# Performance work log

Hardware: AMD Instinct MI355X
Metric: run time of the kernel (lower is better)

Reference implementation:

```python
import jax, jax.numpy as jnp
import numpy as np

B, S, D, F, E, K, H = 4, 1024, 512, 2048, 8, 2, 8
HEAD_DIM = D // H


def setup_inputs() -> dict:
    key = jax.random.key(0)
    ks = jax.random.split(key, 8)
    s = 0.02
    return {
        "x": jax.random.normal(ks[0], (B, S, D), jnp.float32),
        "gate_Wk": jax.random.normal(ks[1], (D, D), jnp.float32) * s,
        "gate_bk": jnp.zeros((D,), jnp.float32),
        "expert_queries": jax.random.normal(ks[2], (E, D), jnp.float32),
        "Wqkv": jax.random.normal(ks[3], (E, 3 * D, D), jnp.float32) * s,
        "bqkv": jnp.zeros((E, 3 * D), jnp.float32),
        "Wo": jax.random.normal(ks[4], (E, D, D), jnp.float32) * s,
        "bo": jnp.zeros((E, D), jnp.float32),
        "g1": jnp.ones((E, D), jnp.float32),
        "be1": jnp.zeros((E, D), jnp.float32),
        "W1": jax.random.normal(ks[5], (E, F, D), jnp.float32) * s,
        "bf1": jnp.zeros((E, F), jnp.float32),
        "W2": jax.random.normal(ks[6], (E, D, F), jnp.float32) * s,
        "bf2": jnp.zeros((E, D), jnp.float32),
        "g2": jnp.ones((E, D), jnp.float32),
        "be2": jnp.zeros((E, D), jnp.float32),
    }


def _layernorm(x, g, b):
    m = x.mean(-1, keepdims=True)
    v = ((x - m) ** 2).mean(-1, keepdims=True)
    return (x - m) * jax.lax.rsqrt(v + 1e-5) * g + b


def _expert(x, Wqkv, bqkv, Wo, bo, g1, be1, W1, bf1, W2, bf2, g2, be2):
    # x: [B,S,D]; one ExpertTransformerDecoder block (dropout=0, eval)
    b, s, d = x.shape
    qkv = x @ Wqkv.T + bqkv                      # [B,S,3D]
    q, k, v = jnp.split(qkv, 3, axis=-1)
    to_heads = lambda t: t.reshape(b, s, H, HEAD_DIM).transpose(0, 2, 1, 3)
    q, k, v = to_heads(q), to_heads(k), to_heads(v)
    scale = 1.0 / np.sqrt(HEAD_DIM).astype(np.float32)
    attn = jax.nn.softmax(jnp.einsum('bhqd,bhkd->bhqk', q * scale, k), axis=-1)
    ctx = jnp.einsum('bhqk,bhkd->bhqd', attn, v).transpose(0, 2, 1, 3).reshape(b, s, d)
    ctx = ctx @ Wo.T + bo
    x = _layernorm(x + ctx, g1, be1)
    h = jax.nn.gelu(x @ W1.T + bf1, approximate=False)
    h = jax.nn.gelu(h @ W2.T + bf2, approximate=False)
    return _layernorm(x + h, g2, be2)


def reference(x, gate_Wk, gate_bk, expert_queries, Wqkv, bqkv, Wo, bo,
              g1, be1, W1, bf1, W2, bf2, g2, be2):
    # attention gating: softmax over experts of <key_proj(x), expert_q> * d^-0.5
    keys = x @ gate_Wk.T + gate_bk                      # [B,S,D]
    scores = jnp.einsum('bsd,ed->bse', keys, expert_queries) * (D ** -0.5)
    probs = jax.nn.softmax(scores, axis=-1)             # [B,S,E]
    # top-k mask + renormalize
    _, idx = jax.lax.top_k(probs, K)                    # [B,S,K]
    mask = jax.nn.one_hot(idx, E, dtype=probs.dtype).sum(-2)
    gated = probs * mask
    gated = gated / (gated.sum(-1, keepdims=True) + 1e-9)
    # run all experts densely (as the torch code does), vmapped over E
    eo = jax.vmap(_expert, in_axes=(None,) + (0,) * 12)(
        x, Wqkv, bqkv, Wo, bo, g1, be1, W1, bf1, W2, bf2, g2, be2)  # [E,B,S,D]
    return jnp.einsum('ebsd,bse->bsd', eo, gated)
```

## Files before the change

kernel.cpp:

```cpp
#include <hip/hip_runtime.h>
#include <cstdint>
#include <cmath>

#define Bc 4
#define Sc 1024
#define Dc 512
#define Fc 2048
#define Ec 8
#define Hc 8
#define Mc 4096

typedef unsigned short u16;
typedef __attribute__((ext_vector_type(8))) short bf16x8;
typedef __attribute__((ext_vector_type(4))) float f32x4;

__device__ __forceinline__ float bf2f(u16 u) {
  unsigned v = ((unsigned)u) << 16;
  return __builtin_bit_cast(float, v);
}
__device__ __forceinline__ u16 f2bf(float f) {
  unsigned u = __builtin_bit_cast(unsigned, f);
  unsigned r = 0x7fffu + ((u >> 16) & 1u);
  return (u16)((u + r) >> 16);
}
__device__ __forceinline__ unsigned pack2bf(float a, float b) {
  return (unsigned)f2bf(a) | ((unsigned)f2bf(b) << 16);
}
__device__ __forceinline__ float gelu_f(float x) {
  const float z = 1.5957691216057308f * fmaf(0.044715f * x, x * x, x);
  const float e = __expf(z);
  return x * (1.0f - __builtin_amdgcn_rcpf(e + 1.0f));
}
__device__ __forceinline__ void async16(const void* g, void* l) {
  __builtin_amdgcn_global_load_lds(
      (const __attribute__((address_space(1))) unsigned int*)g,
      (__attribute__((address_space(3))) unsigned int*)l, 16, 0, 0);
}

__global__ __launch_bounds__(256) void cvt5_kernel(const float* __restrict__ p0, u16* __restrict__ q0,
                                                   const float* __restrict__ p1, u16* __restrict__ q1,
                                                   const float* __restrict__ p2, u16* __restrict__ q2,
                                                   const float* __restrict__ p3, u16* __restrict__ q3,
                                                   const float* __restrict__ p4, u16* __restrict__ q4) {
  int bx = blockIdx.x;
  const float* in;
  u16* outp;
  if (bx < 2048) { in = p0; outp = q0; }
  else if (bx < 8192) { in = p1; outp = q1; bx -= 2048; }
  else if (bx < 10240) { in = p2; outp = q2; bx -= 8192; }
  else if (bx < 18432) { in = p3; outp = q3; bx -= 10240; }
  else { in = p4; outp = q4; bx -= 18432; }
  const long long i = ((long long)bx * 256 + threadIdx.x) * 4;
  const float4 v = *(const float4*)(in + i);
  ushort4 o;
  o.x = f2bf(v.x); o.y = f2bf(v.y); o.z = f2bf(v.z); o.w = f2bf(v.w);
  *(ushort4*)(outp + i) = o;
}

__global__ __launch_bounds__(256) void weq_kernel(const float* __restrict__ gWk,
                                                  const float* __restrict__ eq,
                                                  float* __restrict__ weq) {
  __shared__ float red[4][64];
  const int tid = threadIdx.x, wave = tid >> 6, lane = tid & 63;
  const int d = blockIdx.x * 64 + lane;
  const int e = blockIdx.y;
  float acc = 0.f;
  for (int j = wave * 128; j < wave * 128 + 128; ++j)
    acc += gWk[(long long)j * 512 + d] * eq[e * 512 + j];
  red[wave][lane] = acc;
  __syncthreads();
  if (wave == 0)
    weq[e * 512 + d] = red[0][lane] + red[1][lane] + red[2][lane] + red[3][lane];
}
__global__ void beq_kernel(const float* __restrict__ gbk, const float* __restrict__ eq,
                           float* __restrict__ beq) {
  const int wave = threadIdx.x >> 6, lane = threadIdx.x & 63;
  for (int e = wave; e < 8; e += 4) {
    float a = 0.f;
#pragma unroll
    for (int i = 0; i < 8; ++i) a += gbk[lane + 64 * i] * eq[e * 512 + lane + 64 * i];
#pragma unroll
    for (int off = 32; off; off >>= 1) a += __shfl_xor(a, off);
    if (lane == 0) beq[e] = a;
  }
}

__global__ __launch_bounds__(256) void gate_kernel(const float* __restrict__ x,
                                                   const float* __restrict__ weq,
                                                   const float* __restrict__ beq,
                                                   float* __restrict__ gated,
                                                   int* __restrict__ cnt, int* __restrict__ tlist,
                                                   int* __restrict__ pos) {
  const int wave = threadIdx.x >> 6, lane = threadIdx.x & 63;
  const int t = blockIdx.x * 4 + wave;
  const float* xr = x + (long long)t * 512;
  float acc[8] = {};
#pragma unroll
  for (int i = 0; i < 8; ++i) {
    const float xv = xr[lane + 64 * i];
#pragma unroll
    for (int e2 = 0; e2 < 8; ++e2) acc[e2] += xv * weq[e2 * 512 + lane + 64 * i];
  }
#pragma unroll
  for (int e2 = 0; e2 < 8; ++e2)
#pragma unroll
    for (int off = 32; off; off >>= 1) acc[e2] += __shfl_xor(acc[e2], off);
  if (lane == 0) {
    const float scale = 0.044194173824159216f;
    float s[8], mx = -1e30f;
#pragma unroll
    for (int e2 = 0; e2 < 8; ++e2) { s[e2] = (acc[e2] + beq[e2]) * scale; mx = fmaxf(mx, s[e2]); }
    float p[8], sum = 0.f;
#pragma unroll
    for (int e2 = 0; e2 < 8; ++e2) { p[e2] = expf(s[e2] - mx); sum += p[e2]; }
#pragma unroll
    for (int e2 = 0; e2 < 8; ++e2) p[e2] /= sum;
    int i1 = 0;
#pragma unroll
    for (int e2 = 1; e2 < 8; ++e2) if (p[e2] > p[i1]) i1 = e2;
    int i2 = (i1 == 0) ? 1 : 0;
#pragma unroll
    for (int e2 = 0; e2 < 8; ++e2) if (e2 != i1 && e2 != i2 && p[e2] > p[i2]) i2 = e2;
    const float denom = p[i1] + p[i2] + 1e-9f;
#pragma unroll
    for (int e2 = 0; e2 < 8; ++e2)
      gated[t * 8 + e2] = (e2 == i1 || e2 == i2) ? p[e2] / denom : 0.f;
    const int b = t >> 10;
    int s1 = atomicAdd(cnt + i1 * 4 + b, 1);
    tlist[(i1 * 4 + b) * 1024 + s1] = t;
    pos[i1 * 4096 + t] = s1;
    int s2 = atomicAdd(cnt + i2 * 4 + b, 1);
    tlist[(i2 * 4 + b) * 1024 + s2] = t;
    pos[i2 * 4096 + t] = s2;
  }
}

__global__ void pad_kernel(const int* __restrict__ cnt, int* __restrict__ tlist) {
  const int seg = blockIdx.x;
  const int c = cnt[seg];
  const int ce = (c + 127) & ~127;
  const int tpad = (seg & 3) << 10;
  for (int i = c + (int)threadIdx.x; i < ce; i += 128) tlist[seg * 1024 + i] = tpad;
}

__global__ void wl_kernel(const int* __restrict__ cnt, int* __restrict__ wl) {
  const int seg = threadIdx.x;
  if (seg >= 32) return;
  int base = 0;
  for (int s = 0; s < seg; ++s) base += (cnt[s] + 127) >> 7;
  const int nt = (cnt[seg] + 127) >> 7;
  for (int t = 0; t < nt; ++t) wl[base + t] = (seg << 8) | t;
  for (int t = 0; t < 2 * nt; ++t) wl[128 + 2 * base + t] = (seg << 8) | t;
  if (seg == 31) { wl[96] = base + nt; wl[97] = 2 * (base + nt); }
}

template <int GELU, int QKV, int ROUTED, int BK, int GATHER>
__global__ __launch_bounds__(256) void gemm_bf16(
    const u16* __restrict__ A, const u16* __restrict__ Bw, const float* __restrict__ bias,
    u16* __restrict__ Cout, u16* __restrict__ vT, int M, int N, int K, long long Astride,
    long long Bstride, const int* __restrict__ wl, const int* __restrict__ tlist) {
  int e;
  long long bm;
  if (ROUTED) {
    const int total = wl[96];
    if ((int)blockIdx.x >= total) return;
    const int item = wl[blockIdx.x];
    const int seg = item >> 8, tile = item & 255;
    e = seg >> 2;
    bm = ((long long)(seg & 3) << 10) + tile * 128;
  } else {
    e = blockIdx.z;
    bm = (long long)blockIdx.x * 128;
  }
  __shared__ __attribute__((aligned(16))) u16 As[128 * BK];
  __shared__ __attribute__((aligned(16))) u16 Bs[128 * BK];
  const int tid = threadIdx.x;
  const int wave = tid >> 6, lane = tid & 63;
  const long long bn = (long long)blockIdx.y * 128;
  const u16* Ag = A + (long long)e * Astride + bm * K;
  const u16* Bg = Bw + ((long long)e * Bstride + bn) * K;
  constexpr int LPR = BK / 8;
  constexpr int RPI = 512 / BK;
  constexpr int IPW = BK / 16;
  const int lrow = lane / LPR, lpos = lane % LPR;
  const int lm = lane & 15, quad = lane >> 4;
  const int wm = (wave >> 1) * 64, wn = (wave & 1) * 64;
  int tok[IPW];
  if (GATHER) {
    const long long tbase = (long long)e * 4096 + bm;
#pragma unroll
    for (int i = 0; i < IPW; ++i) {
      const int gi = wave * IPW + i;
      tok[i] = tlist[tbase + gi * RPI + lrow];
    }
  }
  f32x4 acc[4][4] = {};
  for (int kk = 0; kk < K; kk += BK) {
    __syncthreads();
#pragma unroll
    for (int i = 0; i < IPW; ++i) {
      const int gi = wave * IPW + i;
      const int row = gi * RPI + lrow;
      const int sc = lpos ^ (row & 7);
      if (GATHER)
        async16(A + (long long)tok[i] * K + kk + sc * 8, &As[gi * 512]);
      else
        async16(Ag + (long long)row * K + kk + sc * 8, &As[gi * 512]);
      async16(Bg + (long long)row * K + kk + sc * 8, &Bs[gi * 512]);
    }
    __syncthreads();
#pragma unroll
    for (int ks = 0; ks < BK / 32; ++ks) {
      bf16x8 af[4], bfr[4];
#pragma unroll
      for (int mi = 0; mi < 4; ++mi) {
        const int row = wm + mi * 16 + lm;
        const int ch = (ks * 4 + quad) ^ (row & 7);
        af[mi] = *(const bf16x8*)(As + row * BK + ch * 8);
      }
#pragma unroll
      for (int nj = 0; nj < 4; ++nj) {
        const int row = wn + nj * 16 + lm;
        const int ch = (ks * 4 + quad) ^ (row & 7);
        bfr[nj] = *(const bf16x8*)(Bs + row * BK + ch * 8);
      }
#pragma unroll
      for (int mi = 0; mi < 4; ++mi)
#pragma unroll
        for (int nj = 0; nj < 4; ++nj)
          acc[mi][nj] = __builtin_amdgcn_mfma_f32_16x16x32_bf16(bfr[nj], af[mi], acc[mi][nj], 0, 0, 0);
    }
  }
  const float* bs = bias + (long long)e * Bstride;
#pragma unroll
  for (int mi = 0; mi < 4; ++mi) {
    const int m = (int)bm + wm + mi * 16 + lm;
#pragma unroll
    for (int nj = 0; nj < 4; ++nj) {
      const int n0 = (int)bn + wn + nj * 16 + quad * 4;
      const float4 bv = *(const float4*)(bs + n0);
      float v0 = acc[mi][nj][0] + bv.x;
      float v1 = acc[mi][nj][1] + bv.y;
      float v2 = acc[mi][nj][2] + bv.z;
      float v3 = acc[mi][nj][3] + bv.w;
      if (GELU) { v0 = gelu_f(v0); v1 = gelu_f(v1); v2 = gelu_f(v2); v3 = gelu_f(v3); }
      if (QKV) {
        if (n0 < 512) {
          uint2 pk; pk.x = pack2bf(v0, v1); pk.y = pack2bf(v2, v3);
          *(uint2*)(Cout + ((long long)e * Mc + m) * 512 + n0) = pk;
        } else {
          const int hh = (n0 - 512) >> 6, dd = (n0 - 512) & 63;
          const int bb = m >> 10, ss = m & 1023;
          u16* vp = vT + ((((long long)e * Bc + bb) * Hc + hh) * 64 + dd) * Sc + ss;
          vp[0] = f2bf(v0); vp[Sc] = f2bf(v1); vp[2 * Sc] = f2bf(v2); vp[3 * Sc] = f2bf(v3);
        }
      } else {
        uint2 pk; pk.x = pack2bf(v0, v1); pk.y = pack2bf(v2, v3);
        *(uint2*)(Cout + ((long long)e * M + m) * N + n0) = pk;
      }
    }
  }
}

__global__ __launch_bounds__(256, 4) void attn_tile(const u16* __restrict__ qb,
                                                    const u16* __restrict__ kb,
                                                    const u16* __restrict__ vT,
                                                    u16* __restrict__ ctx,
                                                    const int* __restrict__ wl) {
  if ((int)blockIdx.x >= wl[97]) return;
  const int item = wl[128 + blockIdx.x];
  const int seg = item >> 8, qt = item & 255;
  const int e = seg >> 2, b = seg & 3, h = blockIdx.y;
  __shared__ __attribute__((aligned(16))) u16 Ks[64 * 64];
  __shared__ __attribute__((aligned(16))) u16 Vs[64 * 64];
  __shared__ __attribute__((aligned(16))) u16 Pl[4][16 * 72];
  const int tid = threadIdx.x, wave = tid >> 6, lane = tid & 63;
  const int lm = lane & 15, quad = lane >> 4;
  const u16* kbase = kb + ((long long)e * Mc + b * Sc) * 512;
  const u16* vbase = vT + ((((long long)e * Bc + b) * Hc + h) * 64) * Sc;
  const int lr = lane >> 3, lc = (lane & 7) ^ lr;
  u16* P = &Pl[wave][0];
  unsigned* P32 = (unsigned*)P;
  const int pwbase = lm * 36 + quad * 2;

  const long long pidx = (long long)seg * 1024 + qt * 64 + wave * 16 + lm;
  bf16x8 aq[2];
#pragma unroll
  for (int ks = 0; ks < 2; ++ks)
    aq[ks] = *(const bf16x8*)(qb + pidx * 512 + h * 64 + ks * 32 + quad * 8);
  f32x4 O[4] = {};
  float lsum = 0.f;

  for (int n0 = 0; n0 < Sc; n0 += 64) {
    __syncthreads();
#pragma unroll
    for (int i = 0; i < 2; ++i) {
      const int rg = wave * 2 + i;
      const int row = rg * 8 + lr;
      async16(kbase + (long long)(n0 + row) * 512 + h * 64 + lc * 8, &Ks[rg * 512]);
      async16(vbase + (long long)row * Sc + n0 + lc * 8, &Vs[rg * 512]);
    }
    __syncthreads();
    f32x4 sT[4];
#pragma unroll
    for (int kj = 0; kj < 4; ++kj) {
      const int row = kj * 16 + lm;
      const bf16x8 k0 = *(const bf16x8*)(Ks + row * 64 + ((quad) ^ (row & 7)) * 8);
      const bf16x8 k1 = *(const bf16x8*)(Ks + row * 64 + ((4 + quad) ^ (row & 7)) * 8);
      f32x4 c = {};
      c = __builtin_amdgcn_mfma_f32_16x16x32_bf16(k0, aq[0], c, 0, 0, 0);
      c = __builtin_amdgcn_mfma_f32_16x16x32_bf16(k1, aq[1], c, 0, 0, 0);
      sT[kj] = c;
    }
#pragma unroll
    for (int kj = 0; kj < 4; ++kj) {
      const float p0 = __expf(sT[kj][0] * 0.125f);
      const float p1 = __expf(sT[kj][1] * 0.125f);
      const float p2 = __expf(sT[kj][2] * 0.125f);
      const float p3 = __expf(sT[kj][3] * 0.125f);
      lsum += (p0 + p1) + (p2 + p3);
      P32[pwbase + kj * 8 + 0] = pack2bf(p0, p1);
      P32[pwbase + kj * 8 + 1] = pack2bf(p2, p3);
    }
    asm volatile("s_waitcnt lgkmcnt(0)" ::: "memory");
    const bf16x8 ap0 = *(const bf16x8*)(P + lm * 72 + quad * 8);
    const bf16x8 ap1 = *(const bf16x8*)(P + lm * 72 + 32 + quad * 8);
#pragma unroll
    for (int d4 = 0; d4 < 4; ++d4) {
      const int row = d4 * 16 + lm;
      const bf16x8 v0 = *(const bf16x8*)(Vs + row * 64 + ((quad) ^ (row & 7)) * 8);
      const bf16x8 v1 = *(const bf16x8*)(Vs + row * 64 + ((4 + quad) ^ (row & 7)) * 8);
      O[d4] = __builtin_amdgcn_mfma_f32_16x16x32_bf16(v0, ap0, O[d4], 0, 0, 0);
      O[d4] = __builtin_amdgcn_mfma_f32_16x16x32_bf16(v1, ap1, O[d4], 0, 0, 0);
    }
  }
  float ls = lsum;
  ls += __shfl_xor(ls, 16);
  ls += __shfl_xor(ls, 32);
  const float inv = 1.0f / ls;
#pragma unroll
  for (int d4 = 0; d4 < 4; ++d4) {
    uint2 pk;
    pk.x = pack2bf(O[d4][0] * inv, O[d4][1] * inv);
    pk.y = pack2bf(O[d4][2] * inv, O[d4][3] * inv);
    *(uint2*)(ctx + pidx * 512 + h * 64 + d4 * 16 + quad * 4) = pk;
  }
}

__global__ __launch_bounds__(256) void ln1_kernel(const float* __restrict__ x,
                                                  const u16* __restrict__ ctxp,
                                                  const float* __restrict__ g1,
                                                  const float* __restrict__ be1,
                                                  u16* __restrict__ x1,
                                                  const int* __restrict__ cnt,
                                                  const int* __restrict__ tlist) {
  const int i = blockIdx.x, b = blockIdx.y, e = blockIdx.z;
  const int seg = (e << 2) + b;
  const int ce = (cnt[seg] + 127) & ~127;
  if (i >= ce) return;
  const long long p = seg * 1024 + i;
  const int t = tlist[p];
  const int tid = threadIdx.x;
  const int wave = tid >> 6, lane = tid & 63;
  __shared__ float sred[4], qred[4];
  const float v0 = x[(long long)t * 512 + tid] + bf2f(ctxp[p * 512 + tid]);
  const float v1 = x[(long long)t * 512 + tid + 256] + bf2f(ctxp[p * 512 + tid + 256]);
  float s = v0 + v1, q = v0 * v0 + v1 * v1;
#pragma unroll
  for (int off = 32; off; off >>= 1) { s += __shfl_xor(s, off); q += __shfl_xor(q, off); }
  if (lane == 0) { sred[wave] = s; qred[wave] = q; }
  __syncthreads();
  s = sred[0] + sred[1] + sred[2] + sred[3];
  q = qred[0] + qred[1] + qred[2] + qred[3];
  const float mean = s * (1.0f / 512.0f);
  const float var = q * (1.0f / 512.0f) - mean * mean;
  const float rstd = rsqrtf(var + 1e-5f);
  x1[p * 512 + tid] = f2bf((v0 - mean) * rstd * g1[e * 512 + tid] + be1[e * 512 + tid]);
  x1[p * 512 + tid + 256] =
      f2bf((v1 - mean) * rstd * g1[e * 512 + tid + 256] + be1[e * 512 + tid + 256]);
}

__global__ __launch_bounds__(256) void ln2_kernel(const u16* __restrict__ x1,
                                                  const u16* __restrict__ h2,
                                                  const float* __restrict__ g2,
                                                  const float* __restrict__ be2,
                                                  const float* __restrict__ gated,
                                                  const int* __restrict__ pos,
                                                  float* __restrict__ out) {
  const int t = blockIdx.x, tid = threadIdx.x;
  const int b = t >> 10;
  const int wave = tid >> 6, lane = tid & 63;
  __shared__ float sred[4], qred[4];
  float o0 = 0.f, o1 = 0.f;
  for (int e = 0; e < 8; ++e) {
    const float wgt = gated[t * 8 + e];
    if (wgt != 0.f) {
      const long long p = ((e << 2) + b) * 1024 + pos[e * 4096 + t];
      const float v0 = bf2f(x1[p * 512 + tid]) + bf2f(h2[p * 512 + tid]);
      const float v1 = bf2f(x1[p * 512 + tid + 256]) + bf2f(h2[p * 512 + tid + 256]);
      float s = v0 + v1, q = v0 * v0 + v1 * v1;
#pragma unroll
      for (int off = 32; off; off >>= 1) { s += __shfl_xor(s, off); q += __shfl_xor(q, off); }
      if (lane == 0) { sred[wave] = s; qred[wave] = q; }
      __syncthreads();
      s = sred[0] + sred[1] + sred[2] + sred[3];
      q = qred[0] + qred[1] + qred[2] + qred[3];
      __syncthreads();
      const float mean = s * (1.0f / 512.0f);
      const float var = q * (1.0f / 512.0f) - mean * mean;
      const float rstd = rsqrtf(var + 1e-5f);
      o0 += wgt * ((v0 - mean) * rstd * g2[e * 512 + tid] + be2[e * 512 + tid]);
      o1 += wgt * ((v1 - mean) * rstd * g2[e * 512 + tid + 256] + be2[e * 512 + tid + 256]);
    }
  }
  out[(long long)t * 512 + tid] = o0;
  out[(long long)t * 512 + tid + 256] = o1;
}

extern "C" void kernel_launch(void* const* d_in, const int* in_sizes, int n_in, void* d_out,
                              int out_size, void* d_ws, size_t ws_size, hipStream_t stream) {
  const float* x    = (const float*)d_in[0];
  const float* gWk  = (const float*)d_in[1];
  const float* gbk  = (const float*)d_in[2];
  const float* eq   = (const float*)d_in[3];
  const float* Wqkv = (const float*)d_in[4];
  const float* bqkv = (const float*)d_in[5];
  const float* Wo   = (const float*)d_in[6];
  const float* bo   = (const float*)d_in[7];
  const float* g1   = (const float*)d_in[8];
  const float* be1  = (const float*)d_in[9];
  const float* W1   = (const float*)d_in[10];
  const float* bf1  = (const float*)d_in[11];
  const float* W2   = (const float*)d_in[12];
  const float* bf2  = (const float*)d_in[13];
  const float* g2   = (const float*)d_in[14];
  const float* be2  = (const float*)d_in[15];
  float* out = (float*)d_out;

  char* wsp = (char*)d_ws;
  size_t off = 0;
  auto take = [&](size_t bytes) -> void* {
    void* p = wsp + off;
    off += (bytes + 255) & ~(size_t)255;
    return p;
  };
  u16* xb    = (u16*)take((size_t)Mc * 512 * 2);
  u16* Wqkvb = (u16*)take((size_t)Ec * 1536 * 512 * 2);
  u16* Wob   = (u16*)take((size_t)Ec * 512 * 512 * 2);
  u16* W1b   = (u16*)take((size_t)Ec * 2048 * 512 * 2);
  u16* W2b   = (u16*)take((size_t)Ec * 512 * 2048 * 2);
  float* weq   = (float*)take(8 * 512 * 4);
  float* beqb  = (float*)take(8 * 4);
  float* gated = (float*)take((size_t)Mc * 8 * 4);
  int* cnt   = (int*)take(32 * 4);
  int* tlist = (int*)take(32 * 1024 * 4);
  int* pos   = (int*)take((size_t)Ec * Mc * 4);
  int* wl    = (int*)take(512 * 4);
  char* big = (char*)take(134217728);
  u16* qb   = (u16*)big;
  u16* kb   = (u16*)(big + 33554432);
  u16* vTb  = (u16*)(big + 67108864);
  u16* ctxp = (u16*)(big + 100663296);
  u16* hb   = (u16*)big;
  u16* ctxb = (u16*)take(33554432);
  u16* h2b  = ctxb;
  u16* x1b  = (u16*)take(33554432);
  (void)in_sizes; (void)n_in; (void)out_size; (void)ws_size;

  cvt5_kernel<<<dim3(26624), dim3(256), 0, stream>>>(x, xb, Wqkv, Wqkvb, Wo, Wob, W1, W1b, W2, W2b);
  hipMemsetAsync(cnt, 0, 32 * 4, stream);
  weq_kernel<<<dim3(8, 8), dim3(256), 0, stream>>>(gWk, eq, weq);
  beq_kernel<<<dim3(1), dim3(256), 0, stream>>>(gbk, eq, beqb);
  gate_kernel<<<dim3(1024), dim3(256), 0, stream>>>(x, weq, beqb, gated, cnt, tlist, pos);
  pad_kernel<<<dim3(32), dim3(128), 0, stream>>>(cnt, tlist);
  wl_kernel<<<dim3(1), dim3(64), 0, stream>>>(cnt, wl);
  gemm_bf16<0, 1, 0, 64, 0><<<dim3(32, 8, 8), dim3(256), 0, stream>>>(
      xb, Wqkvb + 512 * 512, bqkv + 512, kb, vTb, Mc, 1024, 512, 0LL, 1536LL, wl, nullptr);
  gemm_bf16<0, 0, 1, 128, 1><<<dim3(96, 4), dim3(256), 0, stream>>>(
      xb, Wqkvb, bqkv, qb, nullptr, Mc, 512, 512, 0LL, 1536LL, wl, tlist);
  attn_tile<<<dim3(192, 8), dim3(256), 0, stream>>>(qb, kb, vTb, ctxb, wl);
  gemm_bf16<0, 0, 1, 128, 0><<<dim3(96, 4), dim3(256), 0, stream>>>(
      ctxb, Wob, bo, ctxp, nullptr, Mc, 512, 512, (long long)Mc * 512, 512LL, wl, nullptr);
  ln1_kernel<<<dim3(1024, 4, 8), dim3(256), 0, stream>>>(x, ctxp, g1, be1, x1b, cnt, tlist);
  gemm_bf16<1, 0, 1, 128, 0><<<dim3(96, 16), dim3(256), 0, stream>>>(
      x1b, W1b, bf1, hb, nullptr, Mc, 2048, 512, (long long)Mc * 512, 2048LL, wl, nullptr);
  gemm_bf16<1, 0, 1, 128, 0><<<dim3(96, 4), dim3(256), 0, stream>>>(
      hb, W2b, bf2, h2b, nullptr, Mc, 512, 2048, (long long)Mc * 2048, 512LL, wl, nullptr);
  ln2_kernel<<<dim3(4096), dim3(256), 0, stream>>>(x1b, h2b, g2, be2, gated, pos, out);
}
```

Before: 481.8 us.

## Process two query tiles per attention block to reuse K/V loads

The attention kernel now handles 128 query rows per block (two 64-row sub-tiles) instead of 64, so each K/V tile loaded into shared memory and each K fragment read from LDS is reused for twice the query work. The grid is flattened so the 8 heads of one work item sit in adjacent block indices, and the separate doubled worklist is dropped in favour of the 128-row tile list. This halves global K/V traffic and block count, at the cost of more registers per thread (two sets of O accumulators and Q fragments), which may cut occupancy under the 4-blocks launch bound.

```diff
diff --git a/kernel.cpp b/kernel.cpp
--- a/kernel.cpp
+++ b/kernel.cpp
@@ -150,8 +150,7 @@
   for (int s = 0; s < seg; ++s) base += (cnt[s] + 127) >> 7;
   const int nt = (cnt[seg] + 127) >> 7;
   for (int t = 0; t < nt; ++t) wl[base + t] = (seg << 8) | t;
-  for (int t = 0; t < 2 * nt; ++t) wl[128 + 2 * base + t] = (seg << 8) | t;
-  if (seg == 31) { wl[96] = base + nt; wl[97] = 2 * (base + nt); }
+  if (seg == 31) wl[96] = base + nt;
 }
 
 template <int GELU, int QKV, int ROUTED, int BK, int GATHER>
@@ -267,10 +266,11 @@
                                                     const u16* __restrict__ vT,
                                                     u16* __restrict__ ctx,
                                                     const int* __restrict__ wl) {
-  if ((int)blockIdx.x >= wl[97]) return;
-  const int item = wl[128 + blockIdx.x];
-  const int seg = item >> 8, qt = item & 255;
-  const int e = seg >> 2, b = seg & 3, h = blockIdx.y;
+  const int idx = blockIdx.x >> 3, h = blockIdx.x & 7;
+  if (idx >= wl[96]) return;
+  const int item = wl[idx];
+  const int seg = item >> 8, tile = item & 255;
+  const int e = seg >> 2, b = seg & 3;
   __shared__ __attribute__((aligned(16))) u16 Ks[64 * 64];
   __shared__ __attribute__((aligned(16))) u16 Vs[64 * 64];
   __shared__ __attribute__((aligned(16))) u16 Pl[4][16 * 72];
@@ -283,13 +283,15 @@
   unsigned* P32 = (unsigned*)P;
   const int pwbase = lm * 36 + quad * 2;
 
-  const long long pidx = (long long)seg * 1024 + qt * 64 + wave * 16 + lm;
-  bf16x8 aq[2];
-#pragma unroll
-  for (int ks = 0; ks < 2; ++ks)
-    aq[ks] = *(const bf16x8*)(qb + pidx * 512 + h * 64 + ks * 32 + quad * 8);
-  f32x4 O[4] = {};
-  float lsum = 0.f;
+  const long long pidx0 = (long long)seg * 1024 + tile * 128 + wave * 16 + lm;
+  bf16x8 aq[2][2];
+#pragma unroll
+  for (int t = 0; t < 2; ++t)
+#pragma unroll
+    for (int ks = 0; ks < 2; ++ks)
+      aq[t][ks] = *(const bf16x8*)(qb + (pidx0 + t * 64) * 512 + h * 64 + ks * 32 + quad * 8);
+  f32x4 O[2][4] = {};
+  float lsum[2] = {0.f, 0.f};
 
   for (int n0 = 0; n0 < Sc; n0 += 64) {
     __syncthreads();
@@ -301,49 +303,63 @@
       async16(vbase + (long long)row * Sc + n0 + lc * 8, &Vs[rg * 512]);
     }
     __syncthreads();
-    f32x4 sT[4];
+    bf16x8 kf[4][2];
 #pragma unroll
     for (int kj = 0; kj < 4; ++kj) {
       const int row = kj * 16 + lm;
-      const bf16x8 k0 = *(const bf16x8*)(Ks + row * 64 + ((quad) ^ (row & 7)) * 8);
-      const bf16x8 k1 = *(const bf16x8*)(Ks + row * 64 + ((4 + quad) ^ (row & 7)) * 8);
-      f32x4 c = {};
-      c = __builtin_amdgcn_mfma_f32_16x16x32_bf16(k0, aq[0], c, 0, 0, 0);
-      c = __builtin_amdgcn_mfma_f32_16x16x32_bf16(k1, aq[1], c, 0, 0, 0);
-      sT[kj] = c;
-    }
-#pragma unroll
-    for (int kj = 0; kj < 4; ++kj) {
-      const float p0 = __expf(sT[kj][0] * 0.125f);
-      const float p1 = __expf(sT[kj][1] * 0.125f);
-      const float p2 = __expf(sT[kj][2] * 0.125f);
-      const float p3 = __expf(sT[kj][3] * 0.125f);
-      lsum += (p0 + p1) + (p2 + p3);
-      P32[pwbase + kj * 8 + 0] = pack2bf(p0, p1);
-      P32[pwbase + kj * 8 + 1] = pack2bf(p2, p3);
-    }
-    asm volatile("s_waitcnt lgkmcnt(0)" ::: "memory");
-    const bf16x8 ap0 = *(const bf16x8*)(P + lm * 72 + quad * 8);
-    const bf16x8 ap1 = *(const bf16x8*)(P + lm * 72 + 32 + quad * 8);
+      kf[kj][0] = *(const bf16x8*)(Ks + row * 64 + ((quad) ^ (row & 7)) * 8);
+      kf[kj][1] = *(const bf16x8*)(Ks + row * 64 + ((4 + quad) ^ (row & 7)) * 8);
+    }
+    bf16x8 ap[2][2];
+#pragma unroll
+    for (int t = 0; t < 2; ++t) {
+      f32x4 sT[4];
+#pragma unroll
+      for (int kj = 0; kj < 4; ++kj) {
+        f32x4 c = {};
+        c = __builtin_amdgcn_mfma_f32_16x16x32_bf16(kf[kj][0], aq[t][0], c, 0, 0, 0);
+        c = __builtin_amdgcn_mfma_f32_16x16x32_bf16(kf[kj][1], aq[t][1], c, 0, 0, 0);
+        sT[kj] = c;
+      }
+#pragma unroll
+      for (int kj = 0; kj < 4; ++kj) {
+        const float p0 = __expf(sT[kj][0] * 0.125f);
+        const float p1 = __expf(sT[kj][1] * 0.125f);
+        const float p2 = __expf(sT[kj][2] * 0.125f);
+        const float p3 = __expf(sT[kj][3] * 0.125f);
+        lsum[t] += (p0 + p1) + (p2 + p3);
+        P32[pwbase + kj * 8 + 0] = pack2bf(p0, p1);
+        P32[pwbase + kj * 8 + 1] = pack2bf(p2, p3);
+      }
+      asm volatile("s_waitcnt lgkmcnt(0)" ::: "memory");
+      ap[t][0] = *(const bf16x8*)(P + lm * 72 + quad * 8);
+      ap[t][1] = *(const bf16x8*)(P + lm * 72 + 32 + quad * 8);
+    }
 #pragma unroll
     for (int d4 = 0; d4 < 4; ++d4) {
       const int row = d4 * 16 + lm;
       const bf16x8 v0 = *(const bf16x8*)(Vs + row * 64 + ((quad) ^ (row & 7)) * 8);
       const bf16x8 v1 = *(const bf16x8*)(Vs + row * 64 + ((4 + quad) ^ (row & 7)) * 8);
-      O[d4] = __builtin_amdgcn_mfma_f32_16x16x32_bf16(v0, ap0, O[d4], 0, 0, 0);
-      O[d4] = __builtin_amdgcn_mfma_f32_16x16x32_bf16(v1, ap1, O[d4], 0, 0, 0);
-    }
-  }
-  float ls = lsum;
-  ls += __shfl_xor(ls, 16);
-  ls += __shfl_xor(ls, 32);
-  const float inv = 1.0f / ls;
-#pragma unroll
-  for (int d4 = 0; d4 < 4; ++d4) {
-    uint2 pk;
-    pk.x = pack2bf(O[d4][0] * inv, O[d4][1] * inv);
-    pk.y = pack2bf(O[d4][2] * inv, O[d4][3] * inv);
-    *(uint2*)(ctx + pidx * 512 + h * 64 + d4 * 16 + quad * 4) = pk;
+#pragma unroll
+      for (int t = 0; t < 2; ++t) {
+        O[t][d4] = __builtin_amdgcn_mfma_f32_16x16x32_bf16(v0, ap[t][0], O[t][d4], 0, 0, 0);
+        O[t][d4] = __builtin_amdgcn_mfma_f32_16x16x32_bf16(v1, ap[t][1], O[t][d4], 0, 0, 0);
+      }
+    }
+  }
+#pragma unroll
+  for (int t = 0; t < 2; ++t) {
+    float ls = lsum[t];
+    ls += __shfl_xor(ls, 16);
+    ls += __shfl_xor(ls, 32);
+    const float inv = 1.0f / ls;
+#pragma unroll
+    for (int d4 = 0; d4 < 4; ++d4) {
+      uint2 pk;
+      pk.x = pack2bf(O[t][d4][0] * inv, O[t][d4][1] * inv);
+      pk.y = pack2bf(O[t][d4][2] * inv, O[t][d4][3] * inv);
+      *(uint2*)(ctx + (pidx0 + t * 64) * 512 + h * 64 + d4 * 16 + quad * 4) = pk;
+    }
   }
 }
 
@@ -478,7 +494,7 @@
       xb, Wqkvb + 512 * 512, bqkv + 512, kb, vTb, Mc, 1024, 512, 0LL, 1536LL, wl, nullptr);
   gemm_bf16<0, 0, 1, 128, 1><<<dim3(96, 4), dim3(256), 0, stream>>>(
       xb, Wqkvb, bqkv, qb, nullptr, Mc, 512, 512, 0LL, 1536LL, wl, tlist);
-  attn_tile<<<dim3(192, 8), dim3(256), 0, stream>>>(qb, kb, vTb, ctxb, wl);
+  attn_tile<<<dim3(96 * 8), dim3(256), 0, stream>>>(qb, kb, vTb, ctxb, wl);
   gemm_bf16<0, 0, 1, 128, 0><<<dim3(96, 4), dim3(256), 0, stream>>>(
       ctxb, Wob, bo, ctxp, nullptr, Mc, 512, 512, (long long)Mc * 512, 512LL, wl, nullptr);
   ln1_kernel<<<dim3(1024, 4, 8), dim3(256), 0, stream>>>(x, ctxp, g1, be1, x1b, cnt, tlist);
```

Result: no change. 473.1 us (-1.8%).
